# Kernel optimization log

Measured on AMD Instinct MI355X. Metric: run time of the kernel, lower is better.

Reference implementation:

```python
import jax, jax.numpy as jnp
import numpy as np

MODES1 = 64
MODES2 = 64

def _c(t):
    # real view (..., 2) -> complex
    return jax.lax.complex(t[..., 0], t[..., 1])

def _contract_tt(xf, a, b, c, d):
    # xf: (B, Cin, m1, m2) complex
    # a: (1, Cout, r1, 2), b: (r1, Cin, r2, 2), c: (r2, m1, r3, 2), d: (r3, m2, 1, 2)
    ac = _c(a)[0]          # (Cout, r1)
    bc = _c(b)             # (r1, Cin, r2)
    cc = _c(c)             # (r2, m1, r3)
    dc = _c(d)[..., 0]     # (r3, m2)
    o1 = jnp.einsum('jxk,ky,bcxy->jbcxy', cc, dc, xf)   # (r2, B, Cin, m1, m2)
    return jnp.einsum('oi,icj,jbcxy->boxy', ac, bc, o1)  # (B, Cout, m1, m2)

def setup_inputs() -> dict:
    key = jax.random.key(0)
    ks = jax.random.split(key, 9)
    std = 0.02
    inp = {
        'x':  jax.random.normal(ks[0], (4, 128, 256, 256), dtype=jnp.float32),
        'a1': std * jax.random.normal(ks[1], (1, 128, 64, 2), dtype=jnp.float32),
        'b1': std * jax.random.normal(ks[2], (64, 128, 32, 2), dtype=jnp.float32),
        'c1': std * jax.random.normal(ks[3], (32, 64, 32, 2), dtype=jnp.float32),
        'd1': std * jax.random.normal(ks[4], (32, 64, 1, 2), dtype=jnp.float32),
        'a2': std * jax.random.normal(ks[5], (1, 128, 64, 2), dtype=jnp.float32),
        'b2': std * jax.random.normal(ks[6], (64, 128, 32, 2), dtype=jnp.float32),
        'c2': std * jax.random.normal(ks[7], (32, 64, 32, 2), dtype=jnp.float32),
        'd2': std * jax.random.normal(ks[8], (32, 64, 1, 2), dtype=jnp.float32),
    }
    return inp

def reference(x, a1, b1, c1, d1, a2, b2, c2, d2):
    B, Cin, H, W = x.shape
    Cout = a1.shape[1]
    x_ft = jnp.fft.rfft2(x)  # (B, Cin, H, W//2+1) complex64
    out1 = _contract_tt(x_ft[:, :, :MODES1, :MODES2], a1, b1, c1, d1)
    out2 = _contract_tt(x_ft[:, :, -MODES1:, :MODES2], a2, b2, c2, d2)
    out_ft = jnp.zeros((B, Cout, H, W // 2 + 1), dtype=x_ft.dtype)
    out_ft = out_ft.at[:, :, :MODES1, :MODES2].set(out1)
    out_ft = out_ft.at[:, :, -MODES1:, :MODES2].set(out2)
    return jnp.fft.irfft2(out_ft, s=(H, W))
```

## Files before the change

### kernel.cpp

```cpp
#include <hip/hip_runtime.h>
#include <math.h>


#define TWO_PI 6.28318530717958647692f

typedef __attribute__((ext_vector_type(8))) short short8v;
typedef __attribute__((ext_vector_type(4))) float float4v;

namespace {
constexpr size_t P_ = 32768;

constexpr size_t oYT = 0;
constexpr size_t oXF = 16777216;
constexpr size_t oOF = 25165824;
constexpr size_t oBF = 33554432;
constexpr size_t oAF1 = 33587200;
constexpr size_t oAF2 = 33685504;
constexpr size_t oG  = 33792000;
constexpr size_t oEF = oG + 262144;
constexpr size_t WS_FLOATS = oG + 524288;
}

__device__ __forceinline__ unsigned short f2bf(float f) {
    unsigned int u = __float_as_uint(f);
    unsigned int r = (u + 0x7FFFu + ((u >> 16) & 1u)) >> 16;
    return (unsigned short)r;
}
__device__ __forceinline__ float bf2f(unsigned short b) {
    return __uint_as_float(((unsigned int)b) << 16);
}

__global__ __launch_bounds__(256) void k_prepTables(const float* __restrict__ a1,
                                                    const float* __restrict__ a2,
                                                    unsigned short* __restrict__ AF1,
                                                    unsigned short* __restrict__ AF2,
                                                    unsigned short* __restrict__ BF,
                                                    unsigned short* __restrict__ EF,
                                                    unsigned short* __restrict__ AFa) {
    int idx = blockIdx.x * 256 + threadIdx.x;
    if (idx < 196608) {
        int tbl = (idx >= 98304);
        int id = tbl ? (idx - 98304) : idx;
        int e = id & 7, lane = (id >> 3) & 63;
        int pl = id >> 15;
        float ang;
        if (!tbl) {
            int rt = (id >> 9) & 7, kc = (id >> 12) & 7;
            int r = rt * 16 + (lane & 15);
            int s = kc * 32 + 8 * (lane >> 4) + e;
            int kh = r + ((r >= 64) ? 128 : 0);
            int ph = (kh * s) & 255;
            ang = -TWO_PI * (float)ph / 256.0f;
        } else {
            int rt = (id >> 9) & 15, kc = (id >> 13) & 3;
            int r = rt * 16 + (lane & 15);
            int s = kc * 32 + 8 * (lane >> 4) + e;
            int kh = s + ((s >= 64) ? 128 : 0);
            int ph = (kh * r) & 255;
            ang = TWO_PI * (float)ph / 256.0f;
        }
        float sn, cs; sincosf(ang, &sn, &cs);
        float v = (pl == 0) ? cs : ((pl == 1) ? sn : -sn);
        (tbl ? AF2 : AF1)[id] = f2bf(v);
    } else if (idx < 229376) {
        int id = idx - 196608;
        int e = id & 7, lane = (id >> 3) & 63;
        int nt = (id >> 9) & 3, kc = (id >> 11) & 7;
        int pl = id >> 14;
        int kw = nt * 16 + (lane & 15);
        int w = kc * 32 + 8 * (lane >> 4) + e;
        int ph = (w * kw) & 255;
        float ang = -TWO_PI * (float)ph / 256.0f;
        float sn, cs; sincosf(ang, &sn, &cs);
        BF[id] = f2bf((pl == 0) ? cs : sn);
    } else if (idx < 262144) {
        int id = idx - 229376;
        int e = id & 7, lane = (id >> 3) & 63;
        int nt = (id >> 9) & 15, kc = (id >> 13) & 1, pl = id >> 14;
        int w = nt * 16 + (lane & 15);
        int kw = kc * 32 + 8 * (lane >> 4) + e;
        int ph = (kw * w) & 255;
        float ang = TWO_PI * (float)ph / 256.0f;
        float sn, cs; sincosf(ang, &sn, &cs);
        float sc = ((kw == 0) ? 1.0f : 2.0f) / 65536.0f;
        float v = (pl == 0) ? (sc * cs) : (-sc * sn);
        EF[id] = f2bf(v);
    } else {
        int id = idx - 262144;
        int e = id & 7, lane = (id >> 3) & 63;
        int rt = (id >> 9) & 7, kc = (id >> 12) & 1;
        int plreg = id >> 13;
        int reg = plreg / 3, pl = plreg % 3;
        int o = rt * 16 + (lane & 15);
        int i = kc * 32 + 8 * (lane >> 4) + e;
        const float* ap = reg ? a2 : a1;
        float ar = ap[(o * 64 + i) * 2 + 0];
        float ai = ap[(o * 64 + i) * 2 + 1];
        float v = (pl == 0) ? ar : ((pl == 1) ? ai : -ai);
        AFa[id] = f2bf(v);
    }
}

__global__ __launch_bounds__(256) void k_g(const float* __restrict__ c1, const float* __restrict__ d1,
                                           const float* __restrict__ c2, const float* __restrict__ d2,
                                           float2* __restrict__ G) {
    int idx = blockIdx.x * 256 + threadIdx.x;
    int r = idx >> 17;
    int rem = idx & 131071;
    int j = rem >> 12;
    int xy = rem & 4095;
    int xm = xy >> 6, ym = xy & 63;
    const float* cp = r ? c2 : c1;
    const float* dp = r ? d2 : d1;
    float sr = 0.f, si = 0.f;
    for (int kk = 0; kk < 32; ++kk) {
        float cr = cp[((j * 64 + xm) * 32 + kk) * 2 + 0];
        float ci = cp[((j * 64 + xm) * 32 + kk) * 2 + 1];
        float dr = dp[(kk * 64 + ym) * 2 + 0];
        float di = dp[(kk * 64 + ym) * 2 + 1];
        sr = fmaf(cr, dr, fmaf(-ci, di, sr));
        si = fmaf(cr, di, fmaf( ci, dr, si));
    }
    G[(size_t)(r * 32 + j) * 4096 + xy] = make_float2(sr, si);
}

__global__ __launch_bounds__(256) void k_prepBG(const float* __restrict__ b1, const float* __restrict__ b2,
                                                const float2* __restrict__ G,
                                                unsigned short* __restrict__ bA,
                                                unsigned short* __restrict__ gB) {
    size_t idx = (size_t)blockIdx.x * 256 + threadIdx.x;
    if (idx < 1048576) {
        int e     = idx & 7;
        int lane  = (idx >> 3) & 63;
        int c     = (idx >> 9) & 127;
        int itile = (idx >> 16) & 3;
        int reg   = (idx >> 18) & 1;
        int plane = (idx >> 19) & 1;
        int i = itile * 16 + (lane & 15);
        int j = 8 * (lane >> 4) + e;
        const float* bp = reg ? b2 : b1;
        float v = bp[((size_t)(i * 128 + c) * 32 + j) * 2 + plane];
        bA[idx] = f2bf(v);
    } else if (idx < 1048576 + 786432) {
        size_t i2 = idx - 1048576;
        int e     = i2 & 7;
        int lane  = (i2 >> 3) & 63;
        int ytile = (i2 >> 9) & 3;
        int x     = (i2 >> 11) & 63;
        int reg   = (i2 >> 17) & 1;
        int plane = (int)(i2 >> 18);
        int y = ytile * 16 + (lane & 15);
        int j = 8 * (lane >> 4) + e;
        float2 gv = G[(size_t)(reg * 32 + j) * 4096 + x * 64 + y];
        float v = (plane == 0) ? gv.x : ((plane == 1) ? gv.y : -gv.y);
        gB[i2] = f2bf(v);
    }
}

__global__ __launch_bounds__(256) void k_stage1m(const float* __restrict__ x,
                                                 const unsigned short* __restrict__ BF,
                                                 unsigned short* __restrict__ Yt) {
    __shared__ __align__(16) unsigned short es[8192];
    int t = threadIdx.x;
    int wave = t >> 6, lane = t & 63;
    size_t row0 = (size_t)blockIdx.x * 128 + (size_t)wave * 32;
    int colp = lane & 15, rowq = lane >> 4;
    const short8v* esv = (const short8v*)es;

    float4v accR[2][4], accI[2][4];
#pragma unroll
    for (int rt = 0; rt < 2; ++rt)
#pragma unroll
        for (int nt = 0; nt < 4; ++nt) {
            accR[rt][nt] = (float4v){0.f, 0.f, 0.f, 0.f};
            accI[rt][nt] = (float4v){0.f, 0.f, 0.f, 0.f};
        }

    const float* xb0 = x + (row0 + colp) * 256 + 8 * rowq;
    const float* xb1 = xb0 + 16 * 256;
    float4 nv[2][2];
    nv[0][0] = *(const float4*)(xb0);  nv[0][1] = *(const float4*)(xb0 + 4);
    nv[1][0] = *(const float4*)(xb1);  nv[1][1] = *(const float4*)(xb1 + 4);

    const float4* bf4 = (const float4*)BF;
    for (int ph = 0; ph < 4; ++ph) {
        __syncthreads();
        {
#pragma unroll
            for (int i = 0; i < 4; ++i) {
                int idx = t + 256 * i;
                int li  = idx & 63;
                int nt  = (idx >> 6) & 3;
                int kcl = (idx >> 8) & 1;
                int pl  = idx >> 9;
                ((float4*)es)[idx] = bf4[((size_t)(pl * 8 + ph * 2 + kcl) * 4 + nt) * 64 + li];
            }
        }
        __syncthreads();
        for (int kcl = 0; kcl < 2; ++kcl) {
            int kc = ph * 2 + kcl;
            short8v xh[2];
#pragma unroll
            for (int rt = 0; rt < 2; ++rt) {
                float4 v0 = nv[rt][0], v1 = nv[rt][1];
                float vv[8] = {v0.x, v0.y, v0.z, v0.w, v1.x, v1.y, v1.z, v1.w};
#pragma unroll
                for (int j = 0; j < 8; ++j) xh[rt][j] = (short)f2bf(vv[j]);
            }
            if (kc < 7) {
                nv[0][0] = *(const float4*)(xb0 + (kc + 1) * 32);
                nv[0][1] = *(const float4*)(xb0 + (kc + 1) * 32 + 4);
                nv[1][0] = *(const float4*)(xb1 + (kc + 1) * 32);
                nv[1][1] = *(const float4*)(xb1 + (kc + 1) * 32 + 4);
            }
#pragma unroll
            for (int nt = 0; nt < 4; ++nt) {
                short8v Bch = esv[((0 * 2 + kcl) * 4 + nt) * 64 + lane];
                short8v Bsh = esv[((1 * 2 + kcl) * 4 + nt) * 64 + lane];
#pragma unroll
                for (int rt = 0; rt < 2; ++rt) {
                    accR[rt][nt] = __builtin_amdgcn_mfma_f32_16x16x32_bf16(xh[rt], Bch, accR[rt][nt], 0, 0, 0);
                    accI[rt][nt] = __builtin_amdgcn_mfma_f32_16x16x32_bf16(xh[rt], Bsh, accI[rt][nt], 0, 0, 0);
                }
            }
        }
    }

    short* Yts = (short*)Yt;
    const size_t PLY = (size_t)32 * 32768 * 8;
#pragma unroll
    for (int rt = 0; rt < 2; ++rt) {
        size_t xrow0 = row0 + rt * 16 + rowq * 4;
        int h = (int)(xrow0 & 255), bc = (int)(xrow0 >> 8);
        size_t gbase = (size_t)(h >> 3) * 32768;
        int e0 = h & 7;
#pragma unroll
        for (int nt = 0; nt < 4; ++nt) {
            size_t p = (size_t)bc * 64 + nt * 16 + colp;
            size_t off = (gbase + p) * 8 + e0;
            float4v R = accR[rt][nt], I = accI[rt][nt];
            short rh[4], ih[4];
#pragma unroll
            for (int q = 0; q < 4; ++q) {
                rh[q] = (short)f2bf(R[q]);
                ih[q] = (short)f2bf(I[q]);
            }
            *(short4*)&Yts[0 * PLY + off] = make_short4(rh[0], rh[1], rh[2], rh[3]);
            *(short4*)&Yts[1 * PLY + off] = make_short4(ih[0], ih[1], ih[2], ih[3]);
        }
    }
}

template<int S, int RT_W>
__global__ __launch_bounds__(256) void k_cmfma(const unsigned short* __restrict__ AF,
                                               const unsigned short* __restrict__ Bt,
                                               unsigned int* __restrict__ XFh) {
    constexpr int KC = S / 32;
    constexpr int SG = S / 8;
    constexpr int RTOT = RT_W * 4;
    __shared__ __align__(16) unsigned short bs[2 * SG * 16 * 8];
    int t = threadIdx.x;
    int wave = t >> 6, lane = t & 63;
    int rt0 = wave * RT_W;
    int colp = lane & 15, rowq = lane >> 4;
    const short8v* AFv = (const short8v*)AF;
    const short8v* bsv = (const short8v*)bs;
    const size_t PLA = (size_t)KC * RTOT * 64;

    for (int pt = 0; pt < 4; ++pt) {
        int p0 = blockIdx.x * 64 + pt * 16;
        __syncthreads();
        {
            const float4* src = (const float4*)Bt;
            float4* dst = (float4*)bs;
            for (int e = t; e < 2 * SG * 16; e += 256) {
                int pl = e / (SG * 16); int rem = e - pl * (SG * 16);
                int g = rem >> 4, li = rem & 15;
                dst[e] = src[((size_t)pl * SG + g) * 32768 + p0 + li];
            }
        }
        __syncthreads();
        float4v accR[RT_W], accI[RT_W];
#pragma unroll
        for (int rt = 0; rt < RT_W; ++rt) {
            accR[rt] = (float4v){0.f, 0.f, 0.f, 0.f};
            accI[rt] = (float4v){0.f, 0.f, 0.f, 0.f};
        }
#pragma unroll
        for (int kc = 0; kc < KC; ++kc) {
            int gi = kc * 4 + rowq;
            short8v Brh = bsv[((0 * SG + gi) << 4) + colp];
            short8v Bih = bsv[((1 * SG + gi) << 4) + colp];
#pragma unroll
            for (int rt = 0; rt < RT_W; ++rt) {
                size_t ab = ((size_t)kc * RTOT + rt0 + rt) * 64 + lane;
                short8v Ac  = AFv[0 * PLA + ab];
                short8v As  = AFv[1 * PLA + ab];
                short8v Ans = AFv[2 * PLA + ab];
                float4v r_ = accR[rt];
                r_ = __builtin_amdgcn_mfma_f32_16x16x32_bf16(Ac,  Brh, r_, 0, 0, 0);
                r_ = __builtin_amdgcn_mfma_f32_16x16x32_bf16(Ans, Bih, r_, 0, 0, 0);
                accR[rt] = r_;
                float4v i_ = accI[rt];
                i_ = __builtin_amdgcn_mfma_f32_16x16x32_bf16(As, Brh, i_, 0, 0, 0);
                i_ = __builtin_amdgcn_mfma_f32_16x16x32_bf16(Ac, Bih, i_, 0, 0, 0);
                accI[rt] = i_;
            }
        }
#pragma unroll
        for (int rt = 0; rt < RT_W; ++rt) {
            int rbase = (rt0 + rt) * 16 + rowq * 4;
#pragma unroll
            for (int q = 0; q < 4; ++q) {
                unsigned int pw = (unsigned int)f2bf(accR[rt][q])
                                | ((unsigned int)f2bf(accI[rt][q]) << 16);
                XFh[(size_t)(rbase + q) * P_ + p0 + colp] = pw;
            }
        }
    }
}

__global__ __launch_bounds__(256) void k_contract2(const unsigned int* __restrict__ XFh,
                                                   const unsigned short* __restrict__ bA,
                                                   const unsigned short* __restrict__ gB,
                                                   const unsigned short* __restrict__ AFa,
                                                   unsigned int* __restrict__ OFh) {
    __shared__ __align__(16) unsigned int xfs[4][128][16];
    __shared__ __align__(16) unsigned short ts[2 * 8 * 66 * 8];
    int t = threadIdx.x;
    int k = blockIdx.x >> 2;
    int ytile = blockIdx.x & 3;
    int y0 = ytile << 4;
    int reg = (k >= 64) ? 1 : 0;
    int x = k & 63;
    int itile = t >> 6, lane = t & 63;
    int ylane = lane & 15, qg = lane >> 4;

    {
        const uint4* src = (const uint4*)XFh;
        uint4* dst = (uint4*)xfs;
        size_t kbase = ((size_t)k * 32768 + y0) >> 2;
#pragma unroll
        for (int i = 0; i < 8; ++i) {
            int e = t + 256 * i;
            int f4w = e & 3;
            int bc  = e >> 2;
            int b   = bc >> 7, c = bc & 127;
            dst[e] = src[kbase + (size_t)b * 2048 + (size_t)c * 16 + f4w];
        }
    }

    const short8v* gBv = (const short8v*)gB;
    short8v g_r  = gBv[(((size_t)(0 * 2 + reg) * 64 + x) * 4 + ytile) * 64 + lane];
    short8v g_i  = gBv[(((size_t)(1 * 2 + reg) * 64 + x) * 4 + ytile) * 64 + lane];
    short8v g_ni = gBv[(((size_t)(2 * 2 + reg) * 64 + x) * 4 + ytile) * 64 + lane];

    const short8v* bAv = (const short8v*)bA;
    size_t aR = (((size_t)(0 * 2 + reg) * 4 + itile) * 128) * 64 + lane;
    size_t aI = (((size_t)(1 * 2 + reg) * 4 + itile) * 128) * 64 + lane;

    float tr[4][4], ti[4][4];
#pragma unroll
    for (int q = 0; q < 4; ++q)
#pragma unroll
        for (int b = 0; b < 4; ++b) { tr[q][b] = 0.f; ti[q][b] = 0.f; }

    __syncthreads();

#pragma unroll 2
    for (int c = 0; c < 128; ++c) {
        short8v av = bAv[aR + (size_t)c * 64];
        short8v aw = bAv[aI + (size_t)c * 64];
        float4v z4 = {0.f, 0.f, 0.f, 0.f};
        float4v wr = __builtin_amdgcn_mfma_f32_16x16x32_bf16(av, g_r, z4, 0, 0, 0);
        wr = __builtin_amdgcn_mfma_f32_16x16x32_bf16(aw, g_ni, wr, 0, 0, 0);
        float4v wi = __builtin_amdgcn_mfma_f32_16x16x32_bf16(av, g_i, z4, 0, 0, 0);
        wi = __builtin_amdgcn_mfma_f32_16x16x32_bf16(aw, g_r, wi, 0, 0, 0);
#pragma unroll
        for (int b = 0; b < 4; ++b) {
            unsigned int xw = xfs[b][c][ylane];
            float xr = bf2f((unsigned short)(xw & 0xFFFFu));
            float xi = bf2f((unsigned short)(xw >> 16));
#pragma unroll
            for (int q = 0; q < 4; ++q) {
                tr[q][b] = fmaf(wr[q], xr, fmaf(-wi[q], xi, tr[q][b]));
                ti[q][b] = fmaf(wr[q], xi, fmaf( wi[q], xr, ti[q][b]));
            }
        }
    }

    {
        int gidx = itile * 2 + (qg >> 1);
        int e0 = (qg & 1) * 4;
#pragma unroll
        for (int b = 0; b < 4; ++b) {
            int n = b * 16 + ylane;
            short rh[4], ih[4];
#pragma unroll
            for (int q = 0; q < 4; ++q) {
                rh[q] = (short)f2bf(tr[q][b]);
                ih[q] = (short)f2bf(ti[q][b]);
            }
            *(short4*)&ts[((0 * 8 + gidx) * 66 + n) * 8 + e0] = make_short4(rh[0], rh[1], rh[2], rh[3]);
            *(short4*)&ts[((1 * 8 + gidx) * 66 + n) * 8 + e0] = make_short4(ih[0], ih[1], ih[2], ih[3]);
        }
    }
    __syncthreads();

    const short8v* tsv = (const short8v*)ts;
    const short8v* AFvE = (const short8v*)(AFa + (size_t)reg * 3 * 2 * 8 * 512);
    const size_t PLAe = 2 * 8 * 64;
    float4v eR[2][4], eI[2][4];
#pragma unroll
    for (int rtl = 0; rtl < 2; ++rtl)
#pragma unroll
        for (int nt = 0; nt < 4; ++nt) {
            eR[rtl][nt] = (float4v){0.f, 0.f, 0.f, 0.f};
            eI[rtl][nt] = (float4v){0.f, 0.f, 0.f, 0.f};
        }
#pragma unroll
    for (int kc = 0; kc < 2; ++kc) {
        int gi = kc * 4 + qg;
        short8v Brh[4], Bih[4];
#pragma unroll
        for (int nt = 0; nt < 4; ++nt) {
            Brh[nt] = tsv[(0 * 8 + gi) * 66 + nt * 16 + ylane];
            Bih[nt] = tsv[(1 * 8 + gi) * 66 + nt * 16 + ylane];
        }
#pragma unroll
        for (int rtl = 0; rtl < 2; ++rtl) {
            size_t ab = ((size_t)kc * 8 + itile * 2 + rtl) * 64 + lane;
            short8v Ar  = AFvE[0 * PLAe + ab];
            short8v Ai  = AFvE[1 * PLAe + ab];
            short8v Ani = AFvE[2 * PLAe + ab];
#pragma unroll
            for (int nt = 0; nt < 4; ++nt) {
                float4v r_ = eR[rtl][nt];
                r_ = __builtin_amdgcn_mfma_f32_16x16x32_bf16(Ar,  Brh[nt], r_, 0, 0, 0);
                r_ = __builtin_amdgcn_mfma_f32_16x16x32_bf16(Ani, Bih[nt], r_, 0, 0, 0);
                eR[rtl][nt] = r_;
                float4v i_ = eI[rtl][nt];
                i_ = __builtin_amdgcn_mfma_f32_16x16x32_bf16(Ai, Brh[nt], i_, 0, 0, 0);
                i_ = __builtin_amdgcn_mfma_f32_16x16x32_bf16(Ar, Bih[nt], i_, 0, 0, 0);
                eI[rtl][nt] = i_;
            }
        }
    }
#pragma unroll
    for (int rtl = 0; rtl < 2; ++rtl) {
        int o0 = (itile * 2 + rtl) * 16 + qg * 4;
#pragma unroll
        for (int nt = 0; nt < 4; ++nt) {
#pragma unroll
            for (int q = 0; q < 4; ++q) {
                unsigned int pw = (unsigned int)f2bf(eR[rtl][nt][q])
                                | ((unsigned int)f2bf(eI[rtl][nt][q]) << 16);
                OFh[(size_t)k * 32768 + (size_t)nt * 8192 + (size_t)(o0 + q) * 64 + y0 + ylane] = pw;
            }
        }
    }
}

__global__ __launch_bounds__(512) void k_ihinv(const unsigned short* __restrict__ AF2,
                                               const unsigned int* __restrict__ OFh,
                                               const unsigned short* __restrict__ EF,
                                               float* __restrict__ out) {
    constexpr int SG = 16, KC = 4, RTOT = 16;
    __shared__ __align__(16) unsigned short zs[2 * 256 * 64];
    __shared__ __align__(16) unsigned short bs[2 * SG * 16 * 8];
    int t = threadIdx.x;
    int wave = t >> 6, lane = t & 63;
    int colp = lane & 15, rowq = lane >> 4;
    int rt0 = wave * 2;
    int bo = blockIdx.x;
    size_t p0 = (size_t)bo * 64;
    const short8v* AFv = (const short8v*)AF2;
    const short8v* bsv = (const short8v*)bs;
    const size_t PLA = (size_t)KC * RTOT * 64;

    for (int pt = 0; pt < 4; ++pt) {
        __syncthreads();
        {
            int li = t & 15, g = (t >> 4) & 15, half = t >> 8;
            int e0 = half * 4;
            short rh[4], ih[4];
#pragma unroll
            for (int j = 0; j < 4; ++j) {
                unsigned int w = OFh[(size_t)(g * 8 + e0 + j) * P_ + p0 + pt * 16 + li];
                rh[j] = (short)(w & 0xFFFFu);
                ih[j] = (short)(w >> 16);
            }
            int base = (g * 16 + li) * 8 + e0;
            *(short4*)&bs[0 * 2048 + base] = make_short4(rh[0], rh[1], rh[2], rh[3]);
            *(short4*)&bs[1 * 2048 + base] = make_short4(ih[0], ih[1], ih[2], ih[3]);
        }
        __syncthreads();
        float4v accR[2], accI[2];
#pragma unroll
        for (int rt = 0; rt < 2; ++rt) {
            accR[rt] = (float4v){0.f, 0.f, 0.f, 0.f};
            accI[rt] = (float4v){0.f, 0.f, 0.f, 0.f};
        }
#pragma unroll
        for (int kc = 0; kc < KC; ++kc) {
            int gi = kc * 4 + rowq;
            short8v Brh = bsv[((0 * SG + gi) << 4) + colp];
            short8v Bih = bsv[((1 * SG + gi) << 4) + colp];
#pragma unroll
            for (int rt = 0; rt < 2; ++rt) {
                size_t ab = ((size_t)kc * RTOT + rt0 + rt) * 64 + lane;
                short8v Ac  = AFv[0 * PLA + ab];
                short8v As  = AFv[1 * PLA + ab];
                short8v Ans = AFv[2 * PLA + ab];
                float4v r_ = accR[rt];
                r_ = __builtin_amdgcn_mfma_f32_16x16x32_bf16(Ac,  Brh, r_, 0, 0, 0);
                r_ = __builtin_amdgcn_mfma_f32_16x16x32_bf16(Ans, Bih, r_, 0, 0, 0);
                accR[rt] = r_;
                float4v i_ = accI[rt];
                i_ = __builtin_amdgcn_mfma_f32_16x16x32_bf16(As, Brh, i_, 0, 0, 0);
                i_ = __builtin_amdgcn_mfma_f32_16x16x32_bf16(Ac, Bih, i_, 0, 0, 0);
                accI[rt] = i_;
            }
        }
#pragma unroll
        for (int rt = 0; rt < 2; ++rt)
#pragma unroll
            for (int q = 0; q < 4; ++q) {
                int h = (rt0 + rt) * 16 + rowq * 4 + q;
                int kwsw = (pt * 16 + colp) ^ ((h & 7) << 3);
                zs[h * 64 + kwsw] = (unsigned short)f2bf(accR[rt][q]);
                zs[16384 + h * 64 + kwsw] = (unsigned short)f2bf(accI[rt][q]);
            }
    }
    __syncthreads();

    const short8v* EFv = (const short8v*)EF;
    for (int nt = 0; nt < 16; ++nt) {
        short8v Er0  = EFv[((0 * 2 + 0) * 16 + nt) * 64 + lane];
        short8v Er1  = EFv[((0 * 2 + 1) * 16 + nt) * 64 + lane];
        short8v nEi0 = EFv[((1 * 2 + 0) * 16 + nt) * 64 + lane];
        short8v nEi1 = EFv[((1 * 2 + 1) * 16 + nt) * 64 + lane];
#pragma unroll
        for (int mtl = 0; mtl < 2; ++mtl) {
            int h0 = (wave * 2 + mtl) * 16;
            int hA = h0 + colp;
            int sw = (hA & 7) << 3;
            short8v Zr0 = *(const short8v*)&zs[hA * 64 + ((8 * rowq) ^ sw)];
            short8v Zr1 = *(const short8v*)&zs[hA * 64 + ((32 + 8 * rowq) ^ sw)];
            short8v Zi0 = *(const short8v*)&zs[16384 + hA * 64 + ((8 * rowq) ^ sw)];
            short8v Zi1 = *(const short8v*)&zs[16384 + hA * 64 + ((32 + 8 * rowq) ^ sw)];
            float4v acc = {0.f, 0.f, 0.f, 0.f};
            acc = __builtin_amdgcn_mfma_f32_16x16x32_bf16(Zr0, Er0,  acc, 0, 0, 0);
            acc = __builtin_amdgcn_mfma_f32_16x16x32_bf16(Zi0, nEi0, acc, 0, 0, 0);
            acc = __builtin_amdgcn_mfma_f32_16x16x32_bf16(Zr1, Er1,  acc, 0, 0, 0);
            acc = __builtin_amdgcn_mfma_f32_16x16x32_bf16(Zi1, nEi1, acc, 0, 0, 0);
            size_t ob = ((size_t)bo * 256 + h0 + rowq * 4) * 256 + nt * 16 + colp;
#pragma unroll
            for (int q = 0; q < 4; ++q)
                out[ob + (size_t)q * 256] = acc[q];
        }
    }
}

extern "C" void kernel_launch(void* const* d_in, const int* in_sizes, int n_in,
                              void* d_out, int out_size, void* d_ws, size_t ws_size,
                              hipStream_t stream) {
    const float* x  = (const float*)d_in[0];
    const float* a1 = (const float*)d_in[1];
    const float* b1 = (const float*)d_in[2];
    const float* c1 = (const float*)d_in[3];
    const float* d1 = (const float*)d_in[4];
    const float* a2 = (const float*)d_in[5];
    const float* b2 = (const float*)d_in[6];
    const float* c2 = (const float*)d_in[7];
    const float* d2 = (const float*)d_in[8];
    float* out = (float*)d_out;
    float* wsf = (float*)d_ws;

    if (ws_size < WS_FLOATS * sizeof(float)) return;

    unsigned short* Yt  = (unsigned short*)(wsf + oYT);
    unsigned int*   XFh = (unsigned int*)(wsf + oXF);
    unsigned int*   OFh = (unsigned int*)(wsf + oOF);
    float2*         G   = (float2*)(wsf + oOF);
    unsigned short* BF  = (unsigned short*)(wsf + oBF);
    unsigned short* AF1 = (unsigned short*)(wsf + oAF1);
    unsigned short* AF2 = (unsigned short*)(wsf + oAF2);
    unsigned short* bA  = (unsigned short*)(wsf + oYT);
    unsigned short* gB  = bA + 1048576;
    unsigned short* AFa = (unsigned short*)(wsf + oG);
    unsigned short* EF  = (unsigned short*)(wsf + oEF);

    k_prepTables<<<1216, 256, 0, stream>>>(a1, a2, AF1, AF2, BF, EF, AFa);
    k_g<<<1024, 256, 0, stream>>>(c1, d1, c2, d2, G);
    k_stage1m<<<1024, 256, 0, stream>>>(x, BF, Yt);
    k_cmfma<256, 2><<<512, 256, 0, stream>>>(AF1, Yt, XFh);
    k_prepBG<<<7168, 256, 0, stream>>>(b1, b2, G, bA, gB);
    k_contract2<<<512, 256, 0, stream>>>(XFh, bA, gB, AFa, OFh);
    k_ihinv<<<512, 512, 0, stream>>>(AF2, OFh, EF, out);

    (void)in_sizes; (void)n_in; (void)out_size;
}
```

Measured before the change: 177.6 us.

## Fuse row-DFT stage and column-DFT MFMA into one kernel via LDS

Merges the first-stage row DFT (k_stage1m) and the second-stage column DFT (k_cmfma) into a single kernel, k_fwd. Each 512-thread block handles one (batch, channel) image and keeps the intermediate bf16 spectrum in shared memory instead of writing Yt to global memory and reading it back. This removes a kernel launch and a large global round trip. In exchange each block uses more LDS and 512 threads, and only 512 blocks are launched, which may lower occupancy and latency hiding.

```diff
diff --git a/kernel.cpp b/kernel.cpp
--- a/kernel.cpp
+++ b/kernel.cpp
@@ -157,14 +157,16 @@
     }
 }
 
-__global__ __launch_bounds__(256) void k_stage1m(const float* __restrict__ x,
-                                                 const unsigned short* __restrict__ BF,
-                                                 unsigned short* __restrict__ Yt) {
+__global__ __launch_bounds__(512) void k_fwd(const float* __restrict__ x,
+                                             const unsigned short* __restrict__ BF,
+                                             const unsigned short* __restrict__ AF1,
+                                             unsigned int* __restrict__ XFh) {
     __shared__ __align__(16) unsigned short es[8192];
+    __shared__ __align__(16) unsigned short ys[2 * 32 * 64 * 8];
     int t = threadIdx.x;
     int wave = t >> 6, lane = t & 63;
-    size_t row0 = (size_t)blockIdx.x * 128 + (size_t)wave * 32;
     int colp = lane & 15, rowq = lane >> 4;
+    int bc = blockIdx.x;
     const short8v* esv = (const short8v*)es;
 
     float4v accR[2][4], accI[2][4];
@@ -176,8 +178,8 @@
             accI[rt][nt] = (float4v){0.f, 0.f, 0.f, 0.f};
         }
 
-    const float* xb0 = x + (row0 + colp) * 256 + 8 * rowq;
-    const float* xb1 = xb0 + 16 * 256;
+    const float* xb0 = x + (size_t)bc * 65536 + (size_t)((2 * wave + 0) * 16 + colp) * 256 + 8 * rowq;
+    const float* xb1 = x + (size_t)bc * 65536 + (size_t)((2 * wave + 1) * 16 + colp) * 256 + 8 * rowq;
     float4 nv[2][2];
     nv[0][0] = *(const float4*)(xb0);  nv[0][1] = *(const float4*)(xb0 + 4);
     nv[1][0] = *(const float4*)(xb1);  nv[1][1] = *(const float4*)(xb1 + 4);
@@ -187,8 +189,8 @@
         __syncthreads();
         {
 #pragma unroll
-            for (int i = 0; i < 4; ++i) {
-                int idx = t + 256 * i;
+            for (int i = 0; i < 2; ++i) {
+                int idx = t + 512 * i;
                 int li  = idx & 63;
                 int nt  = (idx >> 6) & 3;
                 int kcl = (idx >> 8) & 1;
@@ -226,96 +228,71 @@
         }
     }
 
-    short* Yts = (short*)Yt;
-    const size_t PLY = (size_t)32 * 32768 * 8;
-#pragma unroll
-    for (int rt = 0; rt < 2; ++rt) {
-        size_t xrow0 = row0 + rt * 16 + rowq * 4;
-        int h = (int)(xrow0 & 255), bc = (int)(xrow0 >> 8);
-        size_t gbase = (size_t)(h >> 3) * 32768;
-        int e0 = h & 7;
+    {
+#pragma unroll
+        for (int rt = 0; rt < 2; ++rt) {
+            int mt = 2 * wave + rt;
+            int g = mt * 2 + (rowq >> 1);
+            int e0 = (rowq & 1) * 4;
+#pragma unroll
+            for (int nt = 0; nt < 4; ++nt) {
+                int kw = nt * 16 + colp;
+                float4v R = accR[rt][nt], I = accI[rt][nt];
+                short rh[4], ih[4];
+#pragma unroll
+                for (int q = 0; q < 4; ++q) {
+                    rh[q] = (short)f2bf(R[q]);
+                    ih[q] = (short)f2bf(I[q]);
+                }
+                *(short4*)&ys[((0 * 32 + g) * 64 + kw) * 8 + e0] = make_short4(rh[0], rh[1], rh[2], rh[3]);
+                *(short4*)&ys[((1 * 32 + g) * 64 + kw) * 8 + e0] = make_short4(ih[0], ih[1], ih[2], ih[3]);
+            }
+        }
+    }
+    __syncthreads();
+
+    const short8v* AFv = (const short8v*)AF1;
+    const short8v* ysv = (const short8v*)ys;
+    const size_t PLA = (size_t)8 * 8 * 64;
+    float4v eR[4], eI[4];
+#pragma unroll
+    for (int nt = 0; nt < 4; ++nt) {
+        eR[nt] = (float4v){0.f, 0.f, 0.f, 0.f};
+        eI[nt] = (float4v){0.f, 0.f, 0.f, 0.f};
+    }
+#pragma unroll
+    for (int kc2 = 0; kc2 < 8; ++kc2) {
+        int g = kc2 * 4 + rowq;
+        short8v Brh[4], Bih[4];
 #pragma unroll
         for (int nt = 0; nt < 4; ++nt) {
-            size_t p = (size_t)bc * 64 + nt * 16 + colp;
-            size_t off = (gbase + p) * 8 + e0;
-            float4v R = accR[rt][nt], I = accI[rt][nt];
-            short rh[4], ih[4];
-#pragma unroll
-            for (int q = 0; q < 4; ++q) {
-                rh[q] = (short)f2bf(R[q]);
-                ih[q] = (short)f2bf(I[q]);
-            }
-            *(short4*)&Yts[0 * PLY + off] = make_short4(rh[0], rh[1], rh[2], rh[3]);
-            *(short4*)&Yts[1 * PLY + off] = make_short4(ih[0], ih[1], ih[2], ih[3]);
-        }
-    }
-}
-
-template<int S, int RT_W>
-__global__ __launch_bounds__(256) void k_cmfma(const unsigned short* __restrict__ AF,
-                                               const unsigned short* __restrict__ Bt,
-                                               unsigned int* __restrict__ XFh) {
-    constexpr int KC = S / 32;
-    constexpr int SG = S / 8;
-    constexpr int RTOT = RT_W * 4;
-    __shared__ __align__(16) unsigned short bs[2 * SG * 16 * 8];
-    int t = threadIdx.x;
-    int wave = t >> 6, lane = t & 63;
-    int rt0 = wave * RT_W;
-    int colp = lane & 15, rowq = lane >> 4;
-    const short8v* AFv = (const short8v*)AF;
-    const short8v* bsv = (const short8v*)bs;
-    const size_t PLA = (size_t)KC * RTOT * 64;
-
-    for (int pt = 0; pt < 4; ++pt) {
-        int p0 = blockIdx.x * 64 + pt * 16;
-        __syncthreads();
-        {
-            const float4* src = (const float4*)Bt;
-            float4* dst = (float4*)bs;
-            for (int e = t; e < 2 * SG * 16; e += 256) {
-                int pl = e / (SG * 16); int rem = e - pl * (SG * 16);
-                int g = rem >> 4, li = rem & 15;
-                dst[e] = src[((size_t)pl * SG + g) * 32768 + p0 + li];
-            }
-        }
-        __syncthreads();
-        float4v accR[RT_W], accI[RT_W];
-#pragma unroll
-        for (int rt = 0; rt < RT_W; ++rt) {
-            accR[rt] = (float4v){0.f, 0.f, 0.f, 0.f};
-            accI[rt] = (float4v){0.f, 0.f, 0.f, 0.f};
-        }
-#pragma unroll
-        for (int kc = 0; kc < KC; ++kc) {
-            int gi = kc * 4 + rowq;
-            short8v Brh = bsv[((0 * SG + gi) << 4) + colp];
-            short8v Bih = bsv[((1 * SG + gi) << 4) + colp];
-#pragma unroll
-            for (int rt = 0; rt < RT_W; ++rt) {
-                size_t ab = ((size_t)kc * RTOT + rt0 + rt) * 64 + lane;
-                short8v Ac  = AFv[0 * PLA + ab];
-                short8v As  = AFv[1 * PLA + ab];
-                short8v Ans = AFv[2 * PLA + ab];
-                float4v r_ = accR[rt];
-                r_ = __builtin_amdgcn_mfma_f32_16x16x32_bf16(Ac,  Brh, r_, 0, 0, 0);
-                r_ = __builtin_amdgcn_mfma_f32_16x16x32_bf16(Ans, Bih, r_, 0, 0, 0);
-                accR[rt] = r_;
-                float4v i_ = accI[rt];
-                i_ = __builtin_amdgcn_mfma_f32_16x16x32_bf16(As, Brh, i_, 0, 0, 0);
-                i_ = __builtin_amdgcn_mfma_f32_16x16x32_bf16(Ac, Bih, i_, 0, 0, 0);
-                accI[rt] = i_;
-            }
-        }
-#pragma unroll
-        for (int rt = 0; rt < RT_W; ++rt) {
-            int rbase = (rt0 + rt) * 16 + rowq * 4;
-#pragma unroll
-            for (int q = 0; q < 4; ++q) {
-                unsigned int pw = (unsigned int)f2bf(accR[rt][q])
-                                | ((unsigned int)f2bf(accI[rt][q]) << 16);
-                XFh[(size_t)(rbase + q) * P_ + p0 + colp] = pw;
-            }
+            Brh[nt] = ysv[(0 * 32 + g) * 64 + nt * 16 + colp];
+            Bih[nt] = ysv[(1 * 32 + g) * 64 + nt * 16 + colp];
+        }
+        size_t ab = ((size_t)kc2 * 8 + wave) * 64 + lane;
+        short8v Ac  = AFv[0 * PLA + ab];
+        short8v As  = AFv[1 * PLA + ab];
+        short8v Ans = AFv[2 * PLA + ab];
+#pragma unroll
+        for (int nt = 0; nt < 4; ++nt) {
+            float4v r_ = eR[nt];
+            r_ = __builtin_amdgcn_mfma_f32_16x16x32_bf16(Ac,  Brh[nt], r_, 0, 0, 0);
+            r_ = __builtin_amdgcn_mfma_f32_16x16x32_bf16(Ans, Bih[nt], r_, 0, 0, 0);
+            eR[nt] = r_;
+            float4v i_ = eI[nt];
+            i_ = __builtin_amdgcn_mfma_f32_16x16x32_bf16(As, Brh[nt], i_, 0, 0, 0);
+            i_ = __builtin_amdgcn_mfma_f32_16x16x32_bf16(Ac, Bih[nt], i_, 0, 0, 0);
+            eI[nt] = i_;
+        }
+    }
+#pragma unroll
+    for (int nt = 0; nt < 4; ++nt) {
+#pragma unroll
+        for (int q = 0; q < 4; ++q) {
+            int k = wave * 16 + rowq * 4 + q;
+            unsigned int pw = (unsigned int)f2bf(eR[nt][q])
+                            | ((unsigned int)f2bf(eI[nt][q]) << 16);
+            XFh[(size_t)k * P_ + (size_t)bc * 64 + nt * 16 + colp] = pw;
         }
     }
 }
@@ -579,7 +556,6 @@
 
     if (ws_size < WS_FLOATS * sizeof(float)) return;
 
-    unsigned short* Yt  = (unsigned short*)(wsf + oYT);
     unsigned int*   XFh = (unsigned int*)(wsf + oXF);
     unsigned int*   OFh = (unsigned int*)(wsf + oOF);
     float2*         G   = (float2*)(wsf + oOF);
@@ -593,8 +569,7 @@
 
     k_prepTables<<<1216, 256, 0, stream>>>(a1, a2, AF1, AF2, BF, EF, AFa);
     k_g<<<1024, 256, 0, stream>>>(c1, d1, c2, d2, G);
-    k_stage1m<<<1024, 256, 0, stream>>>(x, BF, Yt);
-    k_cmfma<256, 2><<<512, 256, 0, stream>>>(AF1, Yt, XFh);
+    k_fwd<<<512, 512, 0, stream>>>(x, BF, AF1, XFh);
     k_prepBG<<<7168, 256, 0, stream>>>(b1, b2, G, bA, gB);
     k_contract2<<<512, 256, 0, stream>>>(XFh, bA, gB, AFa, OFh);
     k_ihinv<<<512, 512, 0, stream>>>(AF2, OFh, EF, out);
```

After: 155.2 us. 12.6% less time.
